# Kernel tuning notes

Hardware: AMD Instinct MI355X
Metric: run time of the kernel (lower is better)

## Reference

```python
import jax, jax.numpy as jnp
import numpy as np


def setup_inputs() -> dict:
    key = jax.random.key(0)
    B, S, H, D = 2, 2048, 16, 64
    qkv = jax.random.normal(key, (B, S, 3, H, D), dtype=jnp.float32)
    return {"qkv_BxSx3xHxD": qkv}


def reference(qkv_BxSx3xHxD):
    # Two-step TTT with linear inner loop (eval mode: dropout_p = 0).
    q = qkv_BxSx3xHxD[:, :, 0]  # [B,S,H,D]
    k = qkv_BxSx3xHxD[:, :, 1]
    v = qkv_BxSx3xHxD[:, :, 2]
    # First causal linear-attention score matrix.
    a1 = jnp.tril(jnp.einsum('bthd,bshd->bhts', q, k))      # [B,H,S,S]
    # Intermediate output against K.
    o2 = jnp.einsum('bhts,bshd->bhtd', a1, k)                # [B,H,S,D]
    # Second causal score matrix from o2 vs K.
    a2 = jnp.tril(jnp.einsum('bhtd,bshd->bhts', o2, k))      # [B,H,S,S]
    a = 2.0 * a1 - a2                                        # fused correction
    return jnp.einsum('bhts,bshd->bthd', a, v)               # [B,S,H,D]
```

## Files before the change

kernel.cpp:

```cpp
#include <hip/hip_runtime.h>
#include <hip/hip_bf16.h>


typedef __bf16 bf16x8 __attribute__((ext_vector_type(8)));
typedef __bf16 bf16x2 __attribute__((ext_vector_type(2)));
typedef float  f32x4  __attribute__((ext_vector_type(4)));

#define MFMA16(a, b, c) __builtin_amdgcn_mfma_f32_16x16x32_bf16((a), (b), (c), 0, 0, 0)

static constexpr int S  = 2048;
static constexpr int H  = 16;
static constexpr int D  = 64;
static constexpr int RS = 3 * H * D;
static constexpr int BN = 64;
static constexpr int LR = 72;

__global__ __launch_bounds__(256, 2)
void ttt_kernel(const float* __restrict__ qkv, float* __restrict__ out)
{
    __shared__ __bf16 ldsS[128 * LR];
    __shared__ __bf16 ldsK[2][BN * LR];
    __shared__ __bf16 ldsW[2][D  * LR];

    const int tid  = threadIdx.x;
    const int wv   = tid >> 6;
    const int lane = tid & 63;
    const int q    = lane >> 4;
    const int l16  = lane & 15;

    const int i  = (int)blockIdx.x;
    const int p  = (i >> 3) & 15;
    const int bh = (i & 7) + 8 * (i >> 7);
    const int b  = bh >> 4;
    const int h  = bh & 15;
    const int tA = 64 * p;
    const int tB = 64 * (31 - p);
    const int nA = p + 1;
    const int nB = 32 - p;

    const float* baseQ = qkv + (size_t)b * S * RS + h * D;
    const float* baseK = baseQ + H * D;
    const float* baseV = baseQ + 2 * H * D;

    const int r2  = (tid >> 3) * 2;
    const int cb  = (tid & 7) * 8;
    const int cbK = cb ^ (((r2 >> 3) & 1) << 5);

    {
        const int r   = tid >> 1;
        const int gr  = (r < 64) ? (tA + r) : (tB + r - 64);
        const int cbq = (tid & 1) * 32;
        const float* pq = baseQ + (size_t)gr * RS + cbq;
        __bf16* dst = ldsS + r * LR + cbq;
#pragma unroll
        for (int u = 0; u < 4; ++u) {
            f32x4 f0 = *(const f32x4*)(pq + u * 8);
            f32x4 f1 = *(const f32x4*)(pq + u * 8 + 4);
            bf16x8 w;
#pragma unroll
            for (int j = 0; j < 4; ++j) { w[j] = (__bf16)f0[j]; w[4 + j] = (__bf16)f1[j]; }
            *(bf16x8*)(dst + u * 8) = w;
        }
    }

    f32x4 pk[4], pv[4];
    auto loadT = [&](f32x4* dst, const float* base, int s0) {
        const float* pg = base + (size_t)(s0 + r2) * RS + cb;
        dst[0] = *(const f32x4*)(pg);
        dst[1] = *(const f32x4*)(pg + 4);
        dst[2] = *(const f32x4*)(pg + RS);
        dst[3] = *(const f32x4*)(pg + RS + 4);
    };

    auto commit = [&](__bf16* K_, __bf16* W_, const f32x4* src) {
        bf16x8 w0, w1;
#pragma unroll
        for (int j = 0; j < 4; ++j) {
            w0[j] = (__bf16)pk[0][j]; w0[4 + j] = (__bf16)pk[1][j];
            w1[j] = (__bf16)pk[2][j]; w1[4 + j] = (__bf16)pk[3][j];
        }
        *(bf16x8*)(K_ + r2 * LR + cbK)       = w0;
        *(bf16x8*)(K_ + (r2 + 1) * LR + cbK) = w1;
#pragma unroll
        for (int j = 0; j < 8; ++j) {
            const int d = cb + j;
            bf16x2 w;
            w[0] = (__bf16)((j < 4) ? src[0][j & 3] : src[1][j & 3]);
            w[1] = (__bf16)((j < 4) ? src[2][j & 3] : src[3][j & 3]);
            *(bf16x2*)(W_ + d * LR + (r2 ^ (d & 56))) = w;
        }
    };

    loadT(pk, baseK, 0);

    __syncthreads();

    bf16x8 Xf[2][2];
    const int rowA = wv * 16;
    const int rowB = 64 + wv * 16;
#pragma unroll
    for (int kt = 0; kt < 2; ++kt) {
        Xf[0][kt] = *(bf16x8*)(ldsS + (rowA + l16) * LR + kt * 32 + q * 8);
        Xf[1][kt] = *(bf16x8*)(ldsS + (rowB + l16) * LR + kt * 32 + q * 8);
    }
    __bf16* sA = ldsS + rowA * LR;
    __bf16* sB = ldsS + rowB * LR;

    const int rp   = (l16 >> 2) * 8 + (l16 & 3);
    const int kcol = (q * 8) | (((l16 >> 2) & 1) << 5);

    const f32x4 zero4 = {0.f, 0.f, 0.f, 0.f};
    f32x4 Y[2][4];
#pragma unroll
    for (int st = 0; st < 2; ++st)
#pragma unroll
        for (int nd = 0; nd < 4; ++nd) Y[st][nd] = zero4;

    const int tgA = tA + wv * 16 + l16;
    const int tgB = tB + wv * 16 + l16;

    commit(ldsK[0], ldsW[0], pk);
    __syncthreads();

    const int NT = 2 * nB;

    for (int u = 0; u < NT; ++u) {
        const int c    = u & 1;
        const int pass = (u >= nB) ? 1 : 0;
        const int sb   = u - (pass ? nB : 0);
        const bool actA = (sb < nA);

        if (u + 1 < NT) {
            const int np  = (u + 1 >= nB) ? 1 : 0;
            const int nsb = (u + 1) - (np ? nB : 0);
            loadT(pk, baseK, nsb * BN);
            if (np) loadT(pv, baseV, nsb * BN);
        }

        __bf16* K_ = ldsK[c];
        __bf16* W_ = ldsW[c];

        f32x4 PtA[4], PtB[4];
#pragma unroll
        for (int mi = 0; mi < 4; ++mi) { PtA[mi] = zero4; PtB[mi] = zero4; }
#pragma unroll
        for (int kt = 0; kt < 2; ++kt) {
#pragma unroll
            for (int mi = 0; mi < 4; ++mi) {
                bf16x8 kf = *(bf16x8*)(K_
                    + ((mi >> 1) * 32 + (mi & 1) * 4 + rp) * LR
                    + ((kt * 32) ^ kcol));
                PtB[mi] = MFMA16(kf, Xf[1][kt], PtB[mi]);
                if (actA) PtA[mi] = MFMA16(kf, Xf[0][kt], PtA[mi]);
            }
        }

        bf16x8 afA[2], afB[2];
        {
            const bool diagB = (sb == nB - 1);
#pragma unroll
            for (int kt = 0; kt < 2; ++kt) {
                bf16x8 a;
                if (diagB) {
#pragma unroll
                    for (int b2 = 0; b2 < 2; ++b2)
#pragma unroll
                        for (int r = 0; r < 4; ++r) {
                            const int sg = sb * BN + kt * 32 + q * 8 + b2 * 4 + r;
                            a[b2 * 4 + r] = (sg <= tgB) ? (__bf16)PtB[2 * kt + b2][r]
                                                        : (__bf16)0.0f;
                        }
                } else {
#pragma unroll
                    for (int b2 = 0; b2 < 2; ++b2)
#pragma unroll
                        for (int r = 0; r < 4; ++r)
                            a[b2 * 4 + r] = (__bf16)PtB[2 * kt + b2][r];
                }
                afB[kt] = a;
            }
            if (actA) {
                const bool diagA = (sb == nA - 1);
#pragma unroll
                for (int kt = 0; kt < 2; ++kt) {
                    bf16x8 a;
                    if (diagA) {
#pragma unroll
                        for (int b2 = 0; b2 < 2; ++b2)
#pragma unroll
                            for (int r = 0; r < 4; ++r) {
                                const int sg = sb * BN + kt * 32 + q * 8 + b2 * 4 + r;
                                a[b2 * 4 + r] = (sg <= tgA) ? (__bf16)PtA[2 * kt + b2][r]
                                                            : (__bf16)0.0f;
                            }
                    } else {
#pragma unroll
                        for (int b2 = 0; b2 < 2; ++b2)
#pragma unroll
                            for (int r = 0; r < 4; ++r)
                                a[b2 * 4 + r] = (__bf16)PtA[2 * kt + b2][r];
                    }
                    afA[kt] = a;
                }
            }
        }

#pragma unroll
        for (int kt = 0; kt < 2; ++kt) {
#pragma unroll
            for (int nd = 0; nd < 4; ++nd) {
                const int d = l16 + nd * 16;
                bf16x8 wf = *(bf16x8*)(W_ + d * LR + ((kt * 32 + q * 8) ^ (d & 56)));
                Y[1][nd] = MFMA16(afB[kt], wf, Y[1][nd]);
                if (actA) Y[0][nd] = MFMA16(afA[kt], wf, Y[0][nd]);
            }
        }

        if (u == nB - 1) {
#pragma unroll
            for (int st = 0; st < 2; ++st) {
                __bf16* sc = (st == 0) ? sA : sB;
#pragma unroll
                for (int nd = 0; nd < 4; ++nd)
#pragma unroll
                    for (int r = 0; r < 4; ++r)
                        sc[(q * 4 + r) * LR + l16 + nd * 16] = (__bf16)Y[st][nd][r];
#pragma unroll
                for (int kt = 0; kt < 2; ++kt) {
                    bf16x8 of = *(bf16x8*)(sc + l16 * LR + kt * 32 + q * 8);
#pragma unroll
                    for (int j = 0; j < 8; ++j)
                        Xf[st][kt][j] = (__bf16)(2.0f * (float)Xf[st][kt][j] - (float)of[j]);
                }
#pragma unroll
                for (int nd = 0; nd < 4; ++nd) Y[st][nd] = zero4;
            }
        } else if (u == NT - 1) {
#pragma unroll
            for (int st = 0; st < 2; ++st) {
                const int tb = (st == 0) ? tA : tB;
#pragma unroll
                for (int nd = 0; nd < 4; ++nd)
#pragma unroll
                    for (int r = 0; r < 4; ++r) {
                        const int t = tb + wv * 16 + q * 4 + r;
                        const int d = l16 + nd * 16;
                        out[(((size_t)b * S + t) * H + h) * D + d] = Y[st][nd][r];
                    }
            }
        }

        if (u + 1 < NT) {
            commit(ldsK[1 - c], ldsW[1 - c], (u + 1 >= nB) ? pv : pk);
            __syncthreads();
        }
    }
}

extern "C" void kernel_launch(void* const* d_in, const int* in_sizes, int n_in,
                              void* d_out, int out_size, void* d_ws, size_t ws_size,
                              hipStream_t stream)
{
    const float* qkv = (const float*)d_in[0];
    float* out = (float*)d_out;
    ttt_kernel<<<dim3(512), 256, 0, stream>>>(qkv, out);
}
```

Measured before the change: 158.3 us.

## Split paired query tiles into one tile per block with heavy-first scheduling

Replaces the paired-tile scheme (tiles p and 31-p sharing a block) with one 64-row query tile per block. The grid doubles, blocks are ordered longest-first, and the smaller LDS footprint allows three blocks per CU. It also preloads W fragments before the second MFMA group and raises wave priority around the MFMA sections. The cost is that K/V staging is no longer shared across two query tiles, so global loads and conversions increase.

```diff
diff --git a/kernel.cpp b/kernel.cpp
--- a/kernel.cpp
+++ b/kernel.cpp
@@ -15,10 +15,10 @@
 static constexpr int BN = 64;
 static constexpr int LR = 72;
 
-__global__ __launch_bounds__(256, 2)
+__global__ __launch_bounds__(256, 3)
 void ttt_kernel(const float* __restrict__ qkv, float* __restrict__ out)
 {
-    __shared__ __bf16 ldsS[128 * LR];
+    __shared__ __bf16 ldsS[64 * LR];
     __shared__ __bf16 ldsK[2][BN * LR];
     __shared__ __bf16 ldsW[2][D  * LR];
 
@@ -29,14 +29,12 @@
     const int l16  = lane & 15;
 
     const int i  = (int)blockIdx.x;
-    const int p  = (i >> 3) & 15;
-    const int bh = (i & 7) + 8 * (i >> 7);
+    const int p  = 31 - (i >> 5);
+    const int bh = i & 31;
     const int b  = bh >> 4;
     const int h  = bh & 15;
-    const int tA = 64 * p;
-    const int tB = 64 * (31 - p);
-    const int nA = p + 1;
-    const int nB = 32 - p;
+    const int t0 = 64 * p;
+    const int nP = p + 1;
 
     const float* baseQ = qkv + (size_t)b * S * RS + h * D;
     const float* baseK = baseQ + H * D;
@@ -47,13 +45,12 @@
     const int cbK = cb ^ (((r2 >> 3) & 1) << 5);
 
     {
-        const int r   = tid >> 1;
-        const int gr  = (r < 64) ? (tA + r) : (tB + r - 64);
-        const int cbq = (tid & 1) * 32;
-        const float* pq = baseQ + (size_t)gr * RS + cbq;
-        __bf16* dst = ldsS + r * LR + cbq;
-#pragma unroll
-        for (int u = 0; u < 4; ++u) {
+        const int r  = tid >> 2;
+        const int cq = (tid & 3) * 16;
+        const float* pq = baseQ + (size_t)(t0 + r) * RS + cq;
+        __bf16* dst = ldsS + r * LR + cq;
+#pragma unroll
+        for (int u = 0; u < 2; ++u) {
             f32x4 f0 = *(const f32x4*)(pq + u * 8);
             f32x4 f1 = *(const f32x4*)(pq + u * 8 + 4);
             bf16x8 w;
@@ -95,54 +92,46 @@
 
     __syncthreads();
 
-    bf16x8 Xf[2][2];
-    const int rowA = wv * 16;
-    const int rowB = 64 + wv * 16;
-#pragma unroll
-    for (int kt = 0; kt < 2; ++kt) {
-        Xf[0][kt] = *(bf16x8*)(ldsS + (rowA + l16) * LR + kt * 32 + q * 8);
-        Xf[1][kt] = *(bf16x8*)(ldsS + (rowB + l16) * LR + kt * 32 + q * 8);
-    }
-    __bf16* sA = ldsS + rowA * LR;
-    __bf16* sB = ldsS + rowB * LR;
+    bf16x8 Xf[2];
+    const int row0 = wv * 16;
+#pragma unroll
+    for (int kt = 0; kt < 2; ++kt)
+        Xf[kt] = *(bf16x8*)(ldsS + (row0 + l16) * LR + kt * 32 + q * 8);
+    __bf16* sc = ldsS + row0 * LR;
 
     const int rp   = (l16 >> 2) * 8 + (l16 & 3);
     const int kcol = (q * 8) | (((l16 >> 2) & 1) << 5);
 
     const f32x4 zero4 = {0.f, 0.f, 0.f, 0.f};
-    f32x4 Y[2][4];
-#pragma unroll
-    for (int st = 0; st < 2; ++st)
-#pragma unroll
-        for (int nd = 0; nd < 4; ++nd) Y[st][nd] = zero4;
-
-    const int tgA = tA + wv * 16 + l16;
-    const int tgB = tB + wv * 16 + l16;
+    f32x4 Y[4];
+#pragma unroll
+    for (int nd = 0; nd < 4; ++nd) Y[nd] = zero4;
+
+    const int tg = t0 + wv * 16 + l16;
 
     commit(ldsK[0], ldsW[0], pk);
     __syncthreads();
 
-    const int NT = 2 * nB;
+    const int NT = 2 * nP;
 
     for (int u = 0; u < NT; ++u) {
-        const int c    = u & 1;
-        const int pass = (u >= nB) ? 1 : 0;
-        const int sb   = u - (pass ? nB : 0);
-        const bool actA = (sb < nA);
+        const int c  = u & 1;
+        const int sb = (u >= nP) ? (u - nP) : u;
 
         if (u + 1 < NT) {
-            const int np  = (u + 1 >= nB) ? 1 : 0;
-            const int nsb = (u + 1) - (np ? nB : 0);
+            const int np_ = (u + 1 >= nP) ? 1 : 0;
+            const int nsb = (u + 1) - (np_ ? nP : 0);
             loadT(pk, baseK, nsb * BN);
-            if (np) loadT(pv, baseV, nsb * BN);
+            if (np_) loadT(pv, baseV, nsb * BN);
         }
 
         __bf16* K_ = ldsK[c];
         __bf16* W_ = ldsW[c];
 
-        f32x4 PtA[4], PtB[4];
-#pragma unroll
-        for (int mi = 0; mi < 4; ++mi) { PtA[mi] = zero4; PtB[mi] = zero4; }
+        f32x4 Pt[4];
+#pragma unroll
+        for (int mi = 0; mi < 4; ++mi) Pt[mi] = zero4;
+        __builtin_amdgcn_s_setprio(1);
 #pragma unroll
         for (int kt = 0; kt < 2; ++kt) {
 #pragma unroll
@@ -150,108 +139,82 @@
                 bf16x8 kf = *(bf16x8*)(K_
                     + ((mi >> 1) * 32 + (mi & 1) * 4 + rp) * LR
                     + ((kt * 32) ^ kcol));
-                PtB[mi] = MFMA16(kf, Xf[1][kt], PtB[mi]);
-                if (actA) PtA[mi] = MFMA16(kf, Xf[0][kt], PtA[mi]);
-            }
-        }
-
-        bf16x8 afA[2], afB[2];
+                Pt[mi] = MFMA16(kf, Xf[kt], Pt[mi]);
+            }
+        }
+        __builtin_amdgcn_s_setprio(0);
+
+        bf16x8 wfr[2][4];
+#pragma unroll
+        for (int kt = 0; kt < 2; ++kt)
+#pragma unroll
+            for (int nd = 0; nd < 4; ++nd) {
+                const int d = l16 + nd * 16;
+                wfr[kt][nd] = *(bf16x8*)(W_ + d * LR + ((kt * 32 + q * 8) ^ (d & 56)));
+            }
+
+        bf16x8 af[2];
         {
-            const bool diagB = (sb == nB - 1);
+            const bool diag = (sb == nP - 1);
 #pragma unroll
             for (int kt = 0; kt < 2; ++kt) {
                 bf16x8 a;
-                if (diagB) {
+                if (diag) {
 #pragma unroll
                     for (int b2 = 0; b2 < 2; ++b2)
 #pragma unroll
                         for (int r = 0; r < 4; ++r) {
                             const int sg = sb * BN + kt * 32 + q * 8 + b2 * 4 + r;
-                            a[b2 * 4 + r] = (sg <= tgB) ? (__bf16)PtB[2 * kt + b2][r]
-                                                        : (__bf16)0.0f;
+                            a[b2 * 4 + r] = (sg <= tg) ? (__bf16)Pt[2 * kt + b2][r]
+                                                       : (__bf16)0.0f;
                         }
                 } else {
 #pragma unroll
                     for (int b2 = 0; b2 < 2; ++b2)
 #pragma unroll
                         for (int r = 0; r < 4; ++r)
-                            a[b2 * 4 + r] = (__bf16)PtB[2 * kt + b2][r];
+                            a[b2 * 4 + r] = (__bf16)Pt[2 * kt + b2][r];
                 }
-                afB[kt] = a;
-            }
-            if (actA) {
-                const bool diagA = (sb == nA - 1);
-#pragma unroll
-                for (int kt = 0; kt < 2; ++kt) {
-                    bf16x8 a;
-                    if (diagA) {
-#pragma unroll
-                        for (int b2 = 0; b2 < 2; ++b2)
-#pragma unroll
-                            for (int r = 0; r < 4; ++r) {
-                                const int sg = sb * BN + kt * 32 + q * 8 + b2 * 4 + r;
-                                a[b2 * 4 + r] = (sg <= tgA) ? (__bf16)PtA[2 * kt + b2][r]
-                                                            : (__bf16)0.0f;
-                            }
-                    } else {
-#pragma unroll
-                        for (int b2 = 0; b2 < 2; ++b2)
-#pragma unroll
-                            for (int r = 0; r < 4; ++r)
-                                a[b2 * 4 + r] = (__bf16)PtA[2 * kt + b2][r];
-                    }
-                    afA[kt] = a;
+                af[kt] = a;
+            }
+        }
+
+        __builtin_amdgcn_s_setprio(1);
+#pragma unroll
+        for (int kt = 0; kt < 2; ++kt)
+#pragma unroll
+            for (int nd = 0; nd < 4; ++nd)
+                Y[nd] = MFMA16(af[kt], wfr[kt][nd], Y[nd]);
+        __builtin_amdgcn_s_setprio(0);
+
+        if (u == nP - 1) {
+#pragma unroll
+            for (int nd = 0; nd < 4; ++nd)
+#pragma unroll
+                for (int r = 0; r < 4; ++r)
+                    sc[(q * 4 + r) * LR + l16 + nd * 16] = (__bf16)Y[nd][r];
+#pragma unroll
+            for (int kt = 0; kt < 2; ++kt) {
+                bf16x8 of = *(bf16x8*)(sc + l16 * LR + kt * 32 + q * 8);
+#pragma unroll
+                for (int j = 0; j < 8; ++j)
+                    Xf[kt][j] = (__bf16)(2.0f * (float)Xf[kt][j] - (float)of[j]);
+            }
+#pragma unroll
+            for (int nd = 0; nd < 4; ++nd) Y[nd] = zero4;
+        } else if (u == NT - 1) {
+#pragma unroll
+            for (int nd = 0; nd < 4; ++nd)
+#pragma unroll
+                for (int r = 0; r < 4; ++r) {
+                    const int t = t0 + wv * 16 + q * 4 + r;
+                    const int d = l16 + nd * 16;
+                    out[(((size_t)b * S + t) * H + h) * D + d] = Y[nd][r];
                 }
-            }
-        }
-
-#pragma unroll
-        for (int kt = 0; kt < 2; ++kt) {
-#pragma unroll
-            for (int nd = 0; nd < 4; ++nd) {
-                const int d = l16 + nd * 16;
-                bf16x8 wf = *(bf16x8*)(W_ + d * LR + ((kt * 32 + q * 8) ^ (d & 56)));
-                Y[1][nd] = MFMA16(afB[kt], wf, Y[1][nd]);
-                if (actA) Y[0][nd] = MFMA16(afA[kt], wf, Y[0][nd]);
-            }
-        }
-
-        if (u == nB - 1) {
-#pragma unroll
-            for (int st = 0; st < 2; ++st) {
-                __bf16* sc = (st == 0) ? sA : sB;
-#pragma unroll
-                for (int nd = 0; nd < 4; ++nd)
-#pragma unroll
-                    for (int r = 0; r < 4; ++r)
-                        sc[(q * 4 + r) * LR + l16 + nd * 16] = (__bf16)Y[st][nd][r];
-#pragma unroll
-                for (int kt = 0; kt < 2; ++kt) {
-                    bf16x8 of = *(bf16x8*)(sc + l16 * LR + kt * 32 + q * 8);
-#pragma unroll
-                    for (int j = 0; j < 8; ++j)
-                        Xf[st][kt][j] = (__bf16)(2.0f * (float)Xf[st][kt][j] - (float)of[j]);
-                }
-#pragma unroll
-                for (int nd = 0; nd < 4; ++nd) Y[st][nd] = zero4;
-            }
-        } else if (u == NT - 1) {
-#pragma unroll
-            for (int st = 0; st < 2; ++st) {
-                const int tb = (st == 0) ? tA : tB;
-#pragma unroll
-                for (int nd = 0; nd < 4; ++nd)
-#pragma unroll
-                    for (int r = 0; r < 4; ++r) {
-                        const int t = tb + wv * 16 + q * 4 + r;
-                        const int d = l16 + nd * 16;
-                        out[(((size_t)b * S + t) * H + h) * D + d] = Y[st][nd][r];
-                    }
-            }
         }
 
         if (u + 1 < NT) {
-            commit(ldsK[1 - c], ldsW[1 - c], (u + 1 >= nB) ? pv : pk);
+            commit(ldsK[1 - c], ldsW[1 - c], (u + 1 >= nP) ? pv : pk);
             __syncthreads();
         }
     }
@@ -263,5 +226,5 @@
 {
     const float* qkv = (const float*)d_in[0];
     float* out = (float*)d_out;
-    ttt_kernel<<<dim3(512), 256, 0, stream>>>(qkv, out);
+    ttt_kernel<<<dim3(1024), 256, 0, stream>>>(qkv, out);
 }
```

After: 137.3 us. -13.3%, faster.
